# Kernel optimization log

Hardware: AMD Instinct MI355X
Metric: run time of the kernel (lower is better)

## Reference

```python
import jax, jax.numpy as jnp
import numpy as np

NUM_HEADS = 8
NUM_LAYER = 4


def setup_inputs() -> dict:
    key = jax.random.key(0)
    k1, k2, k3, k4, k5, k6, k7 = jax.random.split(key, 7)
    bs, num, C = 2, 2048, 256
    H0 = (jax.random.uniform(k1, (bs, num, num)) < 0.3).astype(jnp.float32)
    vertex_feat = jax.random.normal(k2, (bs, C, num), dtype=jnp.float32)
    edge_feat = jax.random.normal(k3, (bs, C, num), dtype=jnp.float32)
    s = 1.0 / np.sqrt(C)
    # Conv1d(kernel_size=1) weights, squeezed to [C_out, C_in]
    Wq = jax.random.uniform(k4, (C, C), minval=-s, maxval=s, dtype=jnp.float32)
    bq = jax.random.uniform(k5, (C,), minval=-s, maxval=s, dtype=jnp.float32)
    Wk = jax.random.uniform(k6, (C, C), minval=-s, maxval=s, dtype=jnp.float32)
    bk = jax.random.uniform(k7, (C,), minval=-s, maxval=s, dtype=jnp.float32)
    return {"H0": H0, "vertex_feat": vertex_feat, "edge_feat": edge_feat,
            "Wq": Wq, "bq": bq, "Wk": Wk, "bk": bk, "iter": 1}


def reference(H0, vertex_feat, edge_feat, Wq, bq, Wk, bk, iter):
    bs, num, _ = H0.shape
    C = vertex_feat.shape[1]
    h = NUM_HEADS
    d = C // h
    # 1x1 Conv1d == per-position linear; reshape to heads: [bs, h, d, num]
    Q = (jnp.einsum('oc,bcn->bon', Wq, vertex_feat) + bq[None, :, None]).reshape(bs, h, d, num)
    K = (jnp.einsum('oc,bcn->bon', Wk, edge_feat) + bk[None, :, None]).reshape(bs, h, d, num)
    attn = jnp.einsum('bhco,bhci->bhoi', Q, K) / np.sqrt(d)  # [bs, h, num, num]
    # attention_mask = (1 - H0).masked_fill((1-H0).bool(), -1e9)
    m = 1.0 - H0
    m = jnp.where(m != 0, jnp.float32(-1e9), m)
    score = jax.nn.sigmoid(attn + m[:, None, :, :]).sum(axis=1) / h  # [bs, num, num]
    # top-k row thresholding (k static: iter is a python int)
    k = max(1, round(num * 0.1 * (NUM_LAYER - 1 - iter)))
    topk_vals = jax.lax.top_k(score, k)[0]           # sorted descending
    a_min = topk_vals[..., -1:]                      # row-wise k-th largest
    W = jnp.where(score >= a_min, score, jnp.float32(0.0))
    H = jnp.where(W > 0, H0, jnp.float32(0.0))
    # degree normalizations (1e-10 keeps them finite; torch isinf branch is a no-op)
    De_n_1 = (1.0 / (H.sum(axis=1) + 1e-10))[..., None]  # [bs, num, 1]
    Dv_n_1 = (1.0 / (H.sum(axis=2) + 1e-10))[..., None]  # [bs, num, 1]
    # F.normalize(W.sum(dim=1), dim=1): L2 normalize with eps=1e-12
    W_edge = W.sum(axis=1)
    W_edge = W_edge / jnp.maximum(jnp.linalg.norm(W_edge, axis=1, keepdims=True), 1e-12)
    W_edge = W_edge[..., None]  # [bs, num, 1]
    return (H, W, De_n_1, Dv_n_1, W_edge)
```

## Files before the change

kernel.cpp:

```cpp
#include <hip/hip_runtime.h>
#include <math.h>

#define NUM 2048
#define CDIM 256
#define NUM_LAYER 4

typedef _Float16 f16x8 __attribute__((ext_vector_type(8)));
typedef unsigned short u16x8 __attribute__((ext_vector_type(8)));
typedef float f32x4 __attribute__((ext_vector_type(4)));

static __device__ __forceinline__ void split_f16(float x, unsigned short& h,
                                                 unsigned short& l) {
  _Float16 hi = (_Float16)x;
  float r = x - (float)hi;
  _Float16 lo = (_Float16)r;
  h = __builtin_bit_cast(unsigned short, hi);
  l = __builtin_bit_cast(unsigned short, lo);
}

__global__ __launch_bounds__(256) void proj_kernel(
    const float* __restrict__ Wq, const float* __restrict__ bq,
    const float* __restrict__ Wk, const float* __restrict__ bk,
    const float* __restrict__ vf, const float* __restrict__ ef,
    unsigned short* __restrict__ Qhi, unsigned short* __restrict__ Qlo,
    unsigned short* __restrict__ Khi, unsigned short* __restrict__ Klo)
{
  const int z = blockIdx.z;
  const int b = z >> 1, mm2 = z & 1;
  const float* __restrict__ Wmat = mm2 ? Wk : Wq;
  const float* __restrict__ bias = mm2 ? bk : bq;
  const float* __restrict__ x = (mm2 ? ef : vf) + (size_t)b * CDIM * NUM;
  unsigned short* __restrict__ ohi = mm2 ? Khi : Qhi;
  unsigned short* __restrict__ olo = mm2 ? Klo : Qlo;

  const int n0 = blockIdx.x * 64;
  const int o0 = blockIdx.y * 64;
  __shared__ float Xs[32][65];
  __shared__ float Ws[64][33];
  __shared__ float T[64][69];
  const int t = threadIdx.x;
  const int tx = t & 15, ty = t >> 4;

  float acc[4][4];
  #pragma unroll
  for (int a = 0; a < 4; a++)
    #pragma unroll
    for (int c = 0; c < 4; c++) acc[a][c] = 0.0f;

  for (int cc = 0; cc < CDIM; cc += 32) {
    #pragma unroll
    for (int e = 0; e < 2; e++) {
      int f = t * 2 + e;
      int row = f >> 4, c4 = f & 15;
      const float4 v = *(const float4*)(&x[(size_t)(cc + row) * NUM + n0 + c4 * 4]);
      Xs[row][c4*4+0] = v.x; Xs[row][c4*4+1] = v.y;
      Xs[row][c4*4+2] = v.z; Xs[row][c4*4+3] = v.w;
    }
    #pragma unroll
    for (int e = 0; e < 2; e++) {
      int f = t * 2 + e;
      int row = f >> 3, c4 = f & 7;
      const float4 v = *(const float4*)(&Wmat[(size_t)(o0 + row) * CDIM + cc + c4 * 4]);
      Ws[row][c4*4+0] = v.x; Ws[row][c4*4+1] = v.y;
      Ws[row][c4*4+2] = v.z; Ws[row][c4*4+3] = v.w;
    }
    __syncthreads();
    #pragma unroll
    for (int kk = 0; kk < 32; kk++) {
      float xv[4], wv[4];
      #pragma unroll
      for (int j = 0; j < 4; j++) xv[j] = Xs[kk][tx*4+j];
      #pragma unroll
      for (int j = 0; j < 4; j++) wv[j] = Ws[ty*4+j][kk];
      #pragma unroll
      for (int oi = 0; oi < 4; oi++)
        #pragma unroll
        for (int ni = 0; ni < 4; ni++)
          acc[oi][ni] = fmaf(wv[oi], xv[ni], acc[oi][ni]);
    }
    __syncthreads();
  }
  float bb[4];
  #pragma unroll
  for (int oi = 0; oi < 4; oi++) bb[oi] = bias[o0 + ty*4 + oi];
  #pragma unroll
  for (int ni = 0; ni < 4; ni++)
    #pragma unroll
    for (int oi = 0; oi < 4; oi++)
      T[tx*4+ni][ty*4+oi] = acc[oi][ni] + bb[oi];
  __syncthreads();
  const int n_l = t >> 2;
  const int oc  = (t & 3) * 16;
  float xv[16];
  #pragma unroll
  for (int j = 0; j < 16; j++) xv[j] = T[n_l][oc + j];
  unsigned short hi[16], lo[16];
  #pragma unroll
  for (int j = 0; j < 16; j++) split_f16(xv[j], hi[j], lo[j]);
  const size_t gb = ((size_t)b * NUM + n0 + n_l) * CDIM + o0 + oc;
  *(u16x8*)&ohi[gb]   = *(u16x8*)&hi[0];
  *(u16x8*)&ohi[gb+8] = *(u16x8*)&hi[8];
  *(u16x8*)&olo[gb]   = *(u16x8*)&lo[0];
  *(u16x8*)&olo[gb+8] = *(u16x8*)&lo[8];
}

__global__ __launch_bounds__(512, 2) void score_kernel(
    const unsigned short* __restrict__ Qhi, const unsigned short* __restrict__ Qlo,
    const unsigned short* __restrict__ Khi, const unsigned short* __restrict__ Klo,
    const float* __restrict__ H0, float* __restrict__ score)
{
  const int b = blockIdx.z;
  const int i0 = blockIdx.x * 128;
  const int o0 = blockIdx.y * 128;
  const int t = threadIdx.x, lane = t & 63, wave = t >> 6;
  const int m = lane & 15, quad = lane >> 4;
  const int obl = (wave & 1) * 64;
  const int ibl = (wave >> 1) * 32;

  __shared__ unsigned short qsh[2][128][36];
  __shared__ unsigned short ksh[2][128][36];

  const int srow = t >> 2;
  const int schk = (t & 3) * 8;

  f32x4 ssum[4][2];
  #pragma unroll
  for (int a = 0; a < 4; a++)
    #pragma unroll
    for (int c = 0; c < 2; c++) ssum[a][c] = (f32x4){0.f, 0.f, 0.f, 0.f};

  const float SC = -1.4426950408889634f * 0.17677669529663687f;

  u16x8 pq[2], pk[2];
  {
    const size_t go = ((size_t)b * NUM + o0 + srow) * CDIM + schk;
    const size_t gi = ((size_t)b * NUM + i0 + srow) * CDIM + schk;
    pq[0] = *(const u16x8*)&Qhi[go];
    pq[1] = *(const u16x8*)&Qlo[go];
    pk[0] = *(const u16x8*)&Khi[gi];
    pk[1] = *(const u16x8*)&Klo[gi];
  }

  for (int h = 0; h < 8; h++) {
    __syncthreads();
    #pragma unroll
    for (int cp = 0; cp < 2; cp++) {
      *(u16x8*)&qsh[cp][srow][schk] = pq[cp];
      *(u16x8*)&ksh[cp][srow][schk] = pk[cp];
    }
    __syncthreads();
    if (h < 7) {
      const int coff = (h + 1) * 32;
      const size_t go = ((size_t)b * NUM + o0 + srow) * CDIM + coff + schk;
      const size_t gi = ((size_t)b * NUM + i0 + srow) * CDIM + coff + schk;
      pq[0] = *(const u16x8*)&Qhi[go];
      pq[1] = *(const u16x8*)&Qlo[go];
      pk[0] = *(const u16x8*)&Khi[gi];
      pk[1] = *(const u16x8*)&Klo[gi];
    }
    f16x8 a[4][2];
    #pragma unroll
    for (int ot = 0; ot < 4; ot++)
      #pragma unroll
      for (int cp = 0; cp < 2; cp++)
        a[ot][cp] = *(const f16x8*)&qsh[cp][obl + ot*16 + m][quad*8];
    #pragma unroll
    for (int it = 0; it < 2; it++) {
      const f16x8 b0 = *(const f16x8*)&ksh[0][ibl + it*16 + m][quad*8];
      const f16x8 b1 = *(const f16x8*)&ksh[1][ibl + it*16 + m][quad*8];
      #pragma unroll
      for (int ot = 0; ot < 4; ot++) {
        f32x4 c = (f32x4){0.f, 0.f, 0.f, 0.f};
        c = __builtin_amdgcn_mfma_f32_16x16x32_f16(a[ot][0], b0, c, 0, 0, 0);
        c = __builtin_amdgcn_mfma_f32_16x16x32_f16(a[ot][0], b1, c, 0, 0, 0);
        c = __builtin_amdgcn_mfma_f32_16x16x32_f16(a[ot][1], b0, c, 0, 0, 0);
        #pragma unroll
        for (int r = 0; r < 4; r++)
          ssum[ot][it][r] += __builtin_amdgcn_rcpf(1.0f + __builtin_amdgcn_exp2f(c[r] * SC));
      }
    }
  }
  const int ob = o0 + obl, ib = i0 + ibl;
  #pragma unroll
  for (int ot = 0; ot < 4; ot++)
    #pragma unroll
    for (int it = 0; it < 2; it++)
      #pragma unroll
      for (int r = 0; r < 4; r++) {
        const int row = ob + ot*16 + quad*4 + r;
        const int col = ib + it*16 + m;
        const size_t idx = ((size_t)b * NUM + row) * NUM + col;
        score[idx] = H0[idx] * ssum[ot][it][r] * 0.125f;
      }
}

__global__ __launch_bounds__(256) void topk_apply_kernel(
    float* __restrict__ scoreW, float* __restrict__ Hout,
    const int* __restrict__ iterp, float* __restrict__ DvOut)
{
  const int wave = threadIdx.x >> 6, lane = threadIdx.x & 63;
  const int row = blockIdx.x * 4 + wave;
  __shared__ unsigned int hist_all[4][256];
  unsigned int* __restrict__ h = hist_all[wave];
  unsigned int* __restrict__ srow = (unsigned int*)scoreW + (size_t)row * NUM;
  float* __restrict__ Hrow = Hout + (size_t)row * NUM;

  uint4 v[8];
  #pragma unroll
  for (int q = 0; q < 8; q++) v[q] = ((const uint4*)srow)[lane + 64*q];

  const int it = iterp[0];
  int k = (int)((double)NUM * 0.1 * (double)(NUM_LAYER - 1 - it) + 0.5);
  if (k < 1) k = 1;
  if (k > NUM) k = NUM;

  unsigned int prefix = 0;
  unsigned int rem = (unsigned int)k;

  for (int pass = 3; pass >= 0; pass--) {
    const int shift = pass * 8;
    const unsigned int pmask = (pass == 3) ? 0u : (0xFFFFFFFFu << (shift + 8));
    *(uint4*)&h[lane*4] = make_uint4(0u, 0u, 0u, 0u);
    __threadfence_block();
    unsigned int zc = 0;
    #pragma unroll
    for (int q = 0; q < 8; q++) {
      const unsigned int vv[4] = {v[q].x, v[q].y, v[q].z, v[q].w};
      #pragma unroll
      for (int e = 0; e < 4; e++) {
        unsigned int val = vv[e];
        if ((val & pmask) == prefix) {
          unsigned int bin = (val >> shift) & 255u;
          if (bin) atomicAdd(&h[bin], 1u);
          else zc++;
        }
      }
    }
    #pragma unroll
    for (int off = 32; off > 0; off >>= 1) zc += __shfl_down(zc, off, 64);
    if (lane == 0) h[0] = zc;
    __threadfence_block();
    const uint4 T = *(const uint4*)&h[lane*4];
    unsigned int s3 = T.w;
    unsigned int s2 = T.z + s3;
    unsigned int s1 = T.y + s2;
    unsigned int s0 = T.x + s1;
    unsigned int tot = s0;
    #pragma unroll
    for (int off = 1; off < 64; off <<= 1) {
      unsigned int y = __shfl_down(tot, off, 64);
      if (lane + off < 64) tot += y;
    }
    const unsigned int ac = tot - s0;
    const unsigned int cum[4]   = {s0 + ac, s1 + ac, s2 + ac, s3 + ac};
    const unsigned int above[4] = {s1 + ac, s2 + ac, s3 + ac, ac};
    int fq = -1;
    #pragma unroll
    for (int q = 0; q < 4; q++)
      if (cum[q] >= rem && above[q] < rem) fq = q;
    const unsigned long long mask = __ballot(fq >= 0);
    const int src = (int)(__ffsll((long long)mask) - 1);
    const unsigned int selbin = (fq >= 0) ? (unsigned int)(lane*4 + fq) : 0u;
    const unsigned int nrem   = (fq >= 0) ? (rem - above[fq]) : 0u;
    const unsigned int sel = (unsigned int)__shfl((int)selbin, src, 64);
    rem = (unsigned int)__shfl((int)nrem, src, 64);
    prefix |= (sel << shift);
  }

  const unsigned int amin = prefix;
  float cnt = 0.0f;
  #pragma unroll
  for (int q = 0; q < 8; q++) {
    unsigned int w0 = (v[q].x >= amin) ? v[q].x : 0u;
    unsigned int w1 = (v[q].y >= amin) ? v[q].y : 0u;
    unsigned int w2 = (v[q].z >= amin) ? v[q].z : 0u;
    unsigned int w3 = (v[q].w >= amin) ? v[q].w : 0u;
    float h0 = (w0 != 0u) ? 1.0f : 0.0f;
    float h1 = (w1 != 0u) ? 1.0f : 0.0f;
    float h2 = (w2 != 0u) ? 1.0f : 0.0f;
    float h3 = (w3 != 0u) ? 1.0f : 0.0f;
    cnt += h0 + h1 + h2 + h3;
    ((uint4*)srow)[lane + 64*q] = make_uint4(w0, w1, w2, w3);
    ((float4*)Hrow)[lane + 64*q] = make_float4(h0, h1, h2, h3);
  }
  #pragma unroll
  for (int off = 32; off > 0; off >>= 1) cnt += __shfl_down(cnt, off, 64);
  if (lane == 0) DvOut[row] = 1.0f / (cnt + 1e-10f);
}

__global__ __launch_bounds__(256) void colsum_kernel(
    const float* __restrict__ Wmat,
    float* __restrict__ colH, float* __restrict__ colW)
{
  const int b = blockIdx.z;
  const int i = blockIdx.x * 256 + threadIdx.x;
  const int o0 = blockIdx.y * 64;
  float sh = 0.0f, sw = 0.0f;
  for (int o = 0; o < 64; o++) {
    size_t idx = ((size_t)b * NUM + o0 + o) * NUM + i;
    float w = Wmat[idx];
    sw += w;
    sh += (w > 0.0f) ? 1.0f : 0.0f;
  }
  atomicAdd(&colH[b * NUM + i], sh);
  atomicAdd(&colW[b * NUM + i], sw);
}

__global__ __launch_bounds__(1024) void finalize_kernel(
    const float* __restrict__ colH, const float* __restrict__ colW,
    float* __restrict__ De, float* __restrict__ We)
{
  const int b = blockIdx.x;
  const int t = threadIdx.x;
  float cw[2];
  float sq = 0.0f;
  #pragma unroll
  for (int j = 0; j < 2; j++) {
    int i = t + 1024*j;
    float ch = colH[b * NUM + i];
    De[b * NUM + i] = 1.0f / (ch + 1e-10f);
    cw[j] = colW[b * NUM + i];
    sq += cw[j] * cw[j];
  }
  for (int off = 32; off > 0; off >>= 1) sq += __shfl_down(sq, off, 64);
  __shared__ float red[16];
  __shared__ float s_nrm;
  if ((t & 63) == 0) red[t >> 6] = sq;
  __syncthreads();
  if (t == 0) {
    float tot = 0.0f;
    for (int i2 = 0; i2 < 16; i2++) tot += red[i2];
    s_nrm = fmaxf(sqrtf(tot), 1e-12f);
  }
  __syncthreads();
  #pragma unroll
  for (int j = 0; j < 2; j++)
    We[b * NUM + t + 1024*j] = cw[j] / s_nrm;
}

extern "C" void kernel_launch(void* const* d_in, const int* in_sizes, int n_in,
                              void* d_out, int out_size, void* d_ws, size_t ws_size,
                              hipStream_t stream) {
  const float* H0 = (const float*)d_in[0];
  const float* vf = (const float*)d_in[1];
  const float* ef = (const float*)d_in[2];
  const float* Wq = (const float*)d_in[3];
  const float* bq = (const float*)d_in[4];
  const float* Wk = (const float*)d_in[5];
  const float* bk = (const float*)d_in[6];
  const int* iter = (const int*)d_in[7];

  float* out = (float*)d_out;
  const size_t nH = (size_t)2 * NUM * NUM;
  float* Hout  = out;
  float* Wout  = out + nH;
  float* DeOut = out + 2 * nH;
  float* DvOut = DeOut + 2 * NUM;
  float* WeOut = DvOut + 2 * NUM;

  float* colH = (float*)d_ws;
  float* colW = colH + 2 * NUM;

  const size_t nC = (size_t)2 * NUM * CDIM;
  unsigned short* base = (unsigned short*)Hout;
  unsigned short* Qhi = base;
  unsigned short* Qlo = base + nC;
  unsigned short* Khi = base + 2 * nC;
  unsigned short* Klo = base + 3 * nC;

  hipMemsetAsync(d_ws, 0, (size_t)2 * 2 * NUM * sizeof(float), stream);

  proj_kernel<<<dim3(NUM/64, CDIM/64, 4), 256, 0, stream>>>(
      Wq, bq, Wk, bk, vf, ef, Qhi, Qlo, Khi, Klo);
  score_kernel<<<dim3(NUM/128, NUM/128, 2), 512, 0, stream>>>(
      Qhi, Qlo, Khi, Klo, H0, Wout);
  topk_apply_kernel<<<dim3(NUM/2), 256, 0, stream>>>(Wout, Hout, iter, DvOut);
  colsum_kernel<<<dim3(NUM/256, NUM/64, 2), 256, 0, stream>>>(Wout, colH, colW);
  finalize_kernel<<<dim3(2), 1024, 0, stream>>>(colH, colW, DeOut, WeOut);
}
```

Before: 198.5 us.

## Double-buffer score kernel LDS tiles and move H0 masking into top-k kernel

The score kernel now uses two LDS buffers per head slice, so each iteration needs one barrier instead of two and the next tile is prefetched two heads ahead. The H0 mask multiply is removed from the score epilogue. Instead the top-k kernel reads H0 alongside the score row and zeroes masked entries before the radix select. This doubles LDS use, which may limit occupancy, and adds an H0 read in the top-k kernel while removing it from the score kernel.

```diff
diff --git a/kernel.cpp b/kernel.cpp
--- a/kernel.cpp
+++ b/kernel.cpp
@@ -107,7 +107,7 @@
 __global__ __launch_bounds__(512, 2) void score_kernel(
     const unsigned short* __restrict__ Qhi, const unsigned short* __restrict__ Qlo,
     const unsigned short* __restrict__ Khi, const unsigned short* __restrict__ Klo,
-    const float* __restrict__ H0, float* __restrict__ score)
+    float* __restrict__ score)
 {
   const int b = blockIdx.z;
   const int i0 = blockIdx.x * 128;
@@ -117,11 +117,13 @@
   const int obl = (wave & 1) * 64;
   const int ibl = (wave >> 1) * 32;
 
-  __shared__ unsigned short qsh[2][128][36];
-  __shared__ unsigned short ksh[2][128][36];
+  __shared__ unsigned short qsh[2][2][128][36];
+  __shared__ unsigned short ksh[2][2][128][36];
 
   const int srow = t >> 2;
   const int schk = (t & 3) * 8;
+  const size_t gq = ((size_t)b * NUM + o0 + srow) * CDIM + schk;
+  const size_t gk = ((size_t)b * NUM + i0 + srow) * CDIM + schk;
 
   f32x4 ssum[4][2];
   #pragma unroll
@@ -132,54 +134,59 @@
   const float SC = -1.4426950408889634f * 0.17677669529663687f;
 
   u16x8 pq[2], pk[2];
-  {
-    const size_t go = ((size_t)b * NUM + o0 + srow) * CDIM + schk;
-    const size_t gi = ((size_t)b * NUM + i0 + srow) * CDIM + schk;
-    pq[0] = *(const u16x8*)&Qhi[go];
-    pq[1] = *(const u16x8*)&Qlo[go];
-    pk[0] = *(const u16x8*)&Khi[gi];
-    pk[1] = *(const u16x8*)&Klo[gi];
-  }
+  pq[0] = *(const u16x8*)&Qhi[gq];
+  pq[1] = *(const u16x8*)&Qlo[gq];
+  pk[0] = *(const u16x8*)&Khi[gk];
+  pk[1] = *(const u16x8*)&Klo[gk];
+  *(u16x8*)&qsh[0][0][srow][schk] = pq[0];
+  *(u16x8*)&qsh[0][1][srow][schk] = pq[1];
+  *(u16x8*)&ksh[0][0][srow][schk] = pk[0];
+  *(u16x8*)&ksh[0][1][srow][schk] = pk[1];
+  __syncthreads();
+  pq[0] = *(const u16x8*)&Qhi[gq + 32];
+  pq[1] = *(const u16x8*)&Qlo[gq + 32];
+  pk[0] = *(const u16x8*)&Khi[gk + 32];
+  pk[1] = *(const u16x8*)&Klo[gk + 32];
 
   for (int h = 0; h < 8; h++) {
-    __syncthreads();
-    #pragma unroll
-    for (int cp = 0; cp < 2; cp++) {
-      *(u16x8*)&qsh[cp][srow][schk] = pq[cp];
-      *(u16x8*)&ksh[cp][srow][schk] = pk[cp];
-    }
-    __syncthreads();
-    if (h < 7) {
-      const int coff = (h + 1) * 32;
-      const size_t go = ((size_t)b * NUM + o0 + srow) * CDIM + coff + schk;
-      const size_t gi = ((size_t)b * NUM + i0 + srow) * CDIM + coff + schk;
-      pq[0] = *(const u16x8*)&Qhi[go];
-      pq[1] = *(const u16x8*)&Qlo[go];
-      pk[0] = *(const u16x8*)&Khi[gi];
-      pk[1] = *(const u16x8*)&Klo[gi];
-    }
+    const int c = h & 1;
     f16x8 a[4][2];
     #pragma unroll
     for (int ot = 0; ot < 4; ot++)
       #pragma unroll
       for (int cp = 0; cp < 2; cp++)
-        a[ot][cp] = *(const f16x8*)&qsh[cp][obl + ot*16 + m][quad*8];
+        a[ot][cp] = *(const f16x8*)&qsh[c][cp][obl + ot*16 + m][quad*8];
     #pragma unroll
     for (int it = 0; it < 2; it++) {
-      const f16x8 b0 = *(const f16x8*)&ksh[0][ibl + it*16 + m][quad*8];
-      const f16x8 b1 = *(const f16x8*)&ksh[1][ibl + it*16 + m][quad*8];
+      const f16x8 b0 = *(const f16x8*)&ksh[c][0][ibl + it*16 + m][quad*8];
+      const f16x8 b1 = *(const f16x8*)&ksh[c][1][ibl + it*16 + m][quad*8];
       #pragma unroll
       for (int ot = 0; ot < 4; ot++) {
-        f32x4 c = (f32x4){0.f, 0.f, 0.f, 0.f};
-        c = __builtin_amdgcn_mfma_f32_16x16x32_f16(a[ot][0], b0, c, 0, 0, 0);
-        c = __builtin_amdgcn_mfma_f32_16x16x32_f16(a[ot][0], b1, c, 0, 0, 0);
-        c = __builtin_amdgcn_mfma_f32_16x16x32_f16(a[ot][1], b0, c, 0, 0, 0);
+        f32x4 cc = (f32x4){0.f, 0.f, 0.f, 0.f};
+        cc = __builtin_amdgcn_mfma_f32_16x16x32_f16(a[ot][0], b0, cc, 0, 0, 0);
+        cc = __builtin_amdgcn_mfma_f32_16x16x32_f16(a[ot][0], b1, cc, 0, 0, 0);
+        cc = __builtin_amdgcn_mfma_f32_16x16x32_f16(a[ot][1], b0, cc, 0, 0, 0);
         #pragma unroll
         for (int r = 0; r < 4; r++)
-          ssum[ot][it][r] += __builtin_amdgcn_rcpf(1.0f + __builtin_amdgcn_exp2f(c[r] * SC));
+          ssum[ot][it][r] += __builtin_amdgcn_rcpf(1.0f + __builtin_amdgcn_exp2f(cc[r] * SC));
       }
     }
-  }
+    if (h < 7) {
+      *(u16x8*)&qsh[c^1][0][srow][schk] = pq[0];
+      *(u16x8*)&qsh[c^1][1][srow][schk] = pq[1];
+      *(u16x8*)&ksh[c^1][0][srow][schk] = pk[0];
+      *(u16x8*)&ksh[c^1][1][srow][schk] = pk[1];
+      __syncthreads();
+      if (h < 6) {
+        const size_t co = (size_t)(h + 2) * 32;
+        pq[0] = *(const u16x8*)&Qhi[gq + co];
+        pq[1] = *(const u16x8*)&Qlo[gq + co];
+        pk[0] = *(const u16x8*)&Khi[gk + co];
+        pk[1] = *(const u16x8*)&Klo[gk + co];
+      }
+    }
+  }
+
   const int ob = o0 + obl, ib = i0 + ibl;
   #pragma unroll
   for (int ot = 0; ot < 4; ot++)
@@ -190,24 +197,33 @@
         const int row = ob + ot*16 + quad*4 + r;
         const int col = ib + it*16 + m;
         const size_t idx = ((size_t)b * NUM + row) * NUM + col;
-        score[idx] = H0[idx] * ssum[ot][it][r] * 0.125f;
+        score[idx] = ssum[ot][it][r] * 0.125f;
       }
 }
 
 __global__ __launch_bounds__(256) void topk_apply_kernel(
-    float* __restrict__ scoreW, float* __restrict__ Hout,
-    const int* __restrict__ iterp, float* __restrict__ DvOut)
+    float* __restrict__ scoreW, const float* __restrict__ H0,
+    float* __restrict__ Hout, const int* __restrict__ iterp,
+    float* __restrict__ DvOut)
 {
   const int wave = threadIdx.x >> 6, lane = threadIdx.x & 63;
   const int row = blockIdx.x * 4 + wave;
   __shared__ unsigned int hist_all[4][256];
   unsigned int* __restrict__ h = hist_all[wave];
   unsigned int* __restrict__ srow = (unsigned int*)scoreW + (size_t)row * NUM;
+  const float* __restrict__ h0row = H0 + (size_t)row * NUM;
   float* __restrict__ Hrow = Hout + (size_t)row * NUM;
 
   uint4 v[8];
   #pragma unroll
-  for (int q = 0; q < 8; q++) v[q] = ((const uint4*)srow)[lane + 64*q];
+  for (int q = 0; q < 8; q++) {
+    const uint4 s4 = ((const uint4*)srow)[lane + 64*q];
+    const float4 m4 = ((const float4*)h0row)[lane + 64*q];
+    v[q].x = (m4.x != 0.0f) ? s4.x : 0u;
+    v[q].y = (m4.y != 0.0f) ? s4.y : 0u;
+    v[q].z = (m4.z != 0.0f) ? s4.z : 0u;
+    v[q].w = (m4.w != 0.0f) ? s4.w : 0u;
+  }
 
   const int it = iterp[0];
   int k = (int)((double)NUM * 0.1 * (double)(NUM_LAYER - 1 - it) + 0.5);
@@ -373,8 +389,8 @@
   proj_kernel<<<dim3(NUM/64, CDIM/64, 4), 256, 0, stream>>>(
       Wq, bq, Wk, bk, vf, ef, Qhi, Qlo, Khi, Klo);
   score_kernel<<<dim3(NUM/128, NUM/128, 2), 512, 0, stream>>>(
-      Qhi, Qlo, Khi, Klo, H0, Wout);
-  topk_apply_kernel<<<dim3(NUM/2), 256, 0, stream>>>(Wout, Hout, iter, DvOut);
+      Qhi, Qlo, Khi, Klo, Wout);
+  topk_apply_kernel<<<dim3(NUM/2), 256, 0, stream>>>(Wout, H0, Hout, iter, DvOut);
   colsum_kernel<<<dim3(NUM/256, NUM/64, 2), 256, 0, stream>>>(Wout, colH, colW);
   finalize_kernel<<<dim3(2), 1024, 0, stream>>>(colH, colW, DeOut, WeOut);
 }
```

After: 196.1 us. About the same (-1.2%).
